# Kernel optimization log

Hardware: AMD Instinct MI355X
Metric: run time of the kernel (lower is better)

The kernel has to match this reference:

```python
import jax, jax.numpy as jnp
import numpy as np

B, WORDS, DIM = 16, 32, 256
HEADS, DIM_HEAD = 8, 32
INNER = HEADS * DIM_HEAD  # 256 == DIM -> project_out True
ITER = 3
J = WORDS * HEADS  # input capsules axis


def setup_inputs() -> dict:
    key = jax.random.key(0)
    ks = jax.random.split(key, 6)
    x = jax.random.normal(ks[0], (B, WORDS, DIM), jnp.float32)
    # capsule transform weights: [J, I, E, D] = [words*heads, words, inner, dim_head]
    W = jax.random.normal(ks[1], (J, WORDS, INNER, DIM_HEAD), jnp.float32)
    bias = 0.01 * jax.random.normal(ks[2], (J, WORDS, INNER), jnp.float32)
    Wi = jax.random.normal(ks[3], (INNER, DIM), jnp.float32) / np.sqrt(DIM)
    bi = jnp.zeros((INNER,), jnp.float32)
    Wo = jax.random.normal(ks[4], (DIM, INNER), jnp.float32) / np.sqrt(INNER)
    bo = jnp.zeros((DIM,), jnp.float32)
    return {"x": x, "W": W, "bias": bias, "Wi": Wi, "bi": bi, "Wo": Wo, "bo": bo}


def _squash(s):
    n = jnp.linalg.norm(s, axis=-1, keepdims=True)
    return n / (1.0 + n * n) * s


def reference(x, W, bias, Wi, bi, Wo, bo):
    # inner projection: [B, WORDS, INNER]
    xi = x @ Wi.T + bi
    # 'b n (h d) -> b (n h) d'
    xh = xi.reshape(B, WORDS * HEADS, DIM_HEAD)
    # u_hat[b,j,i,e] = sum_d W[j,i,e,d] * xh[b,j,d]  -> [B, J, WORDS, INNER]
    u_hat = jnp.einsum('jied,bjd->bjie', W, xh) + bias
    u_det = jax.lax.stop_gradient(u_hat)
    b_log = jnp.zeros_like(u_hat)
    v = None
    for i in range(ITER):
        c = jax.nn.softmax(b_log, axis=2)          # over output capsules (words)
        u = u_hat if i == ITER - 1 else u_det       # detach except last iter
        s = jnp.sum(c * u, axis=1, keepdims=True)   # [B,1,WORDS,INNER]
        v = _squash(s)
        if i < ITER - 1:
            b_log = b_log + jnp.sum(u_det * v, axis=3, keepdims=True)
    out = jnp.squeeze(v, 1) @ Wo.T + bo             # [B, WORDS, DIM]
    return out
```

## Files before the change

kernel.cpp:

```cpp
#include <hip/hip_runtime.h>

#define BB   16
#define NW   32
#define DIMM 256
#define DH   32
#define NI   256
#define NJ   256
#define JP   8
#define JG   (NJ / JP)

__global__ void k_proj_in(const float* __restrict__ x, const float* __restrict__ Wi,
                          const float* __restrict__ bi, float* __restrict__ xh) {
    int row = blockIdx.x;
    int k = threadIdx.x;
    __shared__ float xr[DIMM];
    xr[k] = x[(size_t)row * DIMM + k];
    __syncthreads();
    const float4* wi  = (const float4*)(Wi + (size_t)k * DIMM);
    const float4* xr4 = (const float4*)xr;
    float acc = bi[k];
#pragma unroll 8
    for (int m = 0; m < DIMM / 4; ++m) {
        float4 w = wi[m]; float4 xv = xr4[m];
        acc += w.x * xv.x + w.y * xv.y + w.z * xv.z + w.w * xv.w;
    }
    xh[(size_t)row * DIMM + k] = acc;
}

__global__ void k_uhat(const float* __restrict__ W, const float* __restrict__ bias,
                       const float* __restrict__ xh, float* __restrict__ u,
                       float* __restrict__ part) {
    int jg = blockIdx.x >> 5;
    int i  = blockIdx.x & 31;
    int e  = threadIdx.x;
    __shared__ float xs[BB][DH];
    float acc0[BB];
#pragma unroll
    for (int b = 0; b < BB; ++b) acc0[b] = 0.f;

    for (int jj = 0; jj < JP; ++jj) {
        int j = jg * JP + jj;
        __syncthreads();
        for (int t = threadIdx.x; t < BB * DH; t += 256) {
            int b = t >> 5, d = t & 31;
            xs[b][d] = xh[((size_t)b * NJ + j) * DH + d];
        }
        __syncthreads();
        const float4* wp = (const float4*)(W + (((size_t)j * NW + i) * NI + e) * DH);
        float4 w4[8];
#pragma unroll
        for (int q = 0; q < 8; ++q) w4[q] = wp[q];
        const float* w = (const float*)w4;
        float bv = bias[((size_t)j * NW + i) * NI + e];
#pragma unroll
        for (int b = 0; b < BB; ++b) {
            float a = bv;
#pragma unroll
            for (int d = 0; d < DH; ++d) a += w[d] * xs[b][d];
            u[(((size_t)b * NJ + j) * NW + i) * NI + e] = a;
            acc0[b] += a;
        }
    }
#pragma unroll
    for (int b = 0; b < BB; ++b)
        part[(((size_t)b * JG + jg) * NW + i) * NI + e] = acc0[b];
}

__global__ void k_route(const float* __restrict__ u, const float* __restrict__ v,
                        float* __restrict__ b_log, float* __restrict__ part, int accflag) {
    int b  = blockIdx.x / JG;
    int jg = blockIdx.x % JG;
    int tid = threadIdx.x;
    int lane = tid & 63, wave = tid >> 6;
    __shared__ float vs[NW][NI];
    __shared__ float red[NW][4];
    __shared__ float cs[NW];
    for (int t = tid; t < NW * NI; t += 256)
        vs[t >> 8][t & 255] = v[(size_t)b * NW * NI + t];
    __syncthreads();

    float s_acc[NW];
#pragma unroll
    for (int i = 0; i < NW; ++i) s_acc[i] = 0.f;

    for (int jj = 0; jj < JP; ++jj) {
        int j = jg * JP + jj;
        const float* up = u + ((size_t)b * NJ + j) * NW * NI;
        float ur[NW];
#pragma unroll
        for (int i = 0; i < NW; ++i) ur[i] = up[(size_t)i * NI + tid];
#pragma unroll
        for (int i = 0; i < NW; ++i) {
            float p = ur[i] * vs[i][tid];
#pragma unroll
            for (int off = 32; off >= 1; off >>= 1) p += __shfl_down(p, off);
            if (lane == 0) red[i][wave] = p;
        }
        __syncthreads();
        if (tid < NW) {
            float bta = red[tid][0] + red[tid][1] + red[tid][2] + red[tid][3];
            size_t bidx = ((size_t)b * NJ + j) * NW + tid;
            if (accflag) bta += b_log[bidx];
            b_log[bidx] = bta;
            float m = bta;
#pragma unroll
            for (int mask = 16; mask >= 1; mask >>= 1) m = fmaxf(m, __shfl_xor(m, mask));
            float ex = __expf(bta - m);
            float ssum = ex;
#pragma unroll
            for (int mask = 16; mask >= 1; mask >>= 1) ssum += __shfl_xor(ssum, mask);
            cs[tid] = ex / ssum;
        }
        __syncthreads();
#pragma unroll
        for (int i = 0; i < NW; ++i) s_acc[i] += cs[i] * ur[i];
    }
#pragma unroll
    for (int i = 0; i < NW; ++i)
        part[(((size_t)b * JG + jg) * NW + i) * NI + tid] = s_acc[i];
}

__global__ void k_reduce(const float* __restrict__ part, float* __restrict__ v,
                         float scale) {
    int b = blockIdx.x >> 5;
    int i = blockIdx.x & 31;
    int tid = threadIdx.x;
    int lane = tid & 63, wave = tid >> 6;
    float acc = 0.f;
#pragma unroll 8
    for (int g = 0; g < JG; ++g)
        acc += part[(((size_t)b * JG + g) * NW + i) * NI + tid];
    acc *= scale;
    __shared__ float red[4];
    float p = acc * acc;
#pragma unroll
    for (int off = 32; off >= 1; off >>= 1) p += __shfl_down(p, off);
    if (lane == 0) red[wave] = p;
    __syncthreads();
    float n2 = red[0] + red[1] + red[2] + red[3];
    float n = sqrtf(n2);
    float f = n / (1.0f + n2);
    v[((size_t)b * NW + i) * NI + tid] = f * acc;
}

__global__ void k_proj_out(const float* __restrict__ v, const float* __restrict__ Wo,
                           const float* __restrict__ bo, float* __restrict__ out) {
    int row = blockIdx.x;
    int k = threadIdx.x;
    __shared__ float vr[NI];
    vr[k] = v[(size_t)row * NI + k];
    __syncthreads();
    const float4* wo  = (const float4*)(Wo + (size_t)k * NI);
    const float4* vr4 = (const float4*)vr;
    float acc = bo[k];
#pragma unroll 8
    for (int m = 0; m < NI / 4; ++m) {
        float4 w = wo[m]; float4 xv = vr4[m];
        acc += w.x * xv.x + w.y * xv.y + w.z * xv.z + w.w * xv.w;
    }
    out[(size_t)row * DIMM + k] = acc;
}

extern "C" void kernel_launch(void* const* d_in, const int* in_sizes, int n_in,
                              void* d_out, int out_size, void* d_ws, size_t ws_size,
                              hipStream_t stream) {
    const float* x    = (const float*)d_in[0];
    const float* W    = (const float*)d_in[1];
    const float* bias = (const float*)d_in[2];
    const float* Wi   = (const float*)d_in[3];
    const float* bi   = (const float*)d_in[4];
    const float* Wo   = (const float*)d_in[5];
    const float* bo   = (const float*)d_in[6];
    float* out = (float*)d_out;

    float* ws    = (float*)d_ws;
    float* xh    = ws;
    float* u     = ws + 131072;
    float* part  = u + 33554432;
    float* b_log = part + 4194304;
    float* v     = b_log + 131072;

    k_proj_in<<<dim3(BB * NW), dim3(256), 0, stream>>>(x, Wi, bi, xh);
    k_uhat<<<dim3(JG * NW), dim3(256), 0, stream>>>(W, bias, xh, u, part);
    k_reduce<<<dim3(BB * NW), dim3(256), 0, stream>>>(part, v, 1.0f / NW);
    k_route<<<dim3(BB * JG), dim3(256), 0, stream>>>(u, v, b_log, part, 0);
    k_reduce<<<dim3(BB * NW), dim3(256), 0, stream>>>(part, v, 1.0f);
    k_route<<<dim3(BB * JG), dim3(256), 0, stream>>>(u, v, b_log, part, 1);
    k_reduce<<<dim3(BB * NW), dim3(256), 0, stream>>>(part, v, 1.0f);
    k_proj_out<<<dim3(BB * NW), dim3(256), 0, stream>>>(v, Wo, bo, out);
}
```

Baseline: 606.4 us.

## Remap routing threads to (capsule, slice) with vectorized loads and halve JP

The routing kernel now gives each thread a 32-element contiguous slice of one output capsule row. It loads u and v with float4 reads and reduces the dot product over only 8 lanes, replacing the per-capsule 64-wide wave reductions and the 32KB shared-memory copy of v. Every thread recomputes the softmax from shared beta values instead of one wave doing it, which removes one barrier per iteration. JP drops from 8 to 4 to double the number of blocks, which doubles the partial-sum buffer and the work in k_uhat and k_reduce, and the workspace offsets are shifted to match.

After: 579.8 us. 4.4% less time.

```diff
diff --git a/kernel.cpp b/kernel.cpp
--- a/kernel.cpp
+++ b/kernel.cpp
@@ -6,7 +6,7 @@
 #define DH   32
 #define NI   256
 #define NJ   256
-#define JP   8
+#define JP   4
 #define JG   (NJ / JP)
 
 __global__ void k_proj_in(const float* __restrict__ x, const float* __restrict__ Wi,
@@ -70,54 +70,59 @@
                         float* __restrict__ b_log, float* __restrict__ part, int accflag) {
     int b  = blockIdx.x / JG;
     int jg = blockIdx.x % JG;
-    int tid = threadIdx.x;
-    int lane = tid & 63, wave = tid >> 6;
-    __shared__ float vs[NW][NI];
-    __shared__ float red[NW][4];
-    __shared__ float cs[NW];
-    for (int t = tid; t < NW * NI; t += 256)
-        vs[t >> 8][t & 255] = v[(size_t)b * NW * NI + t];
-    __syncthreads();
+    int t  = threadIdx.x;
+    int i  = t >> 3;
+    int h  = t & 7;
+    __shared__ float sh_beta[JP][NW];
 
-    float s_acc[NW];
+    float vr[32];
+    {
+        const float4* vp = (const float4*)(v + ((size_t)b * NW + i) * NI + h * 32);
 #pragma unroll
-    for (int i = 0; i < NW; ++i) s_acc[i] = 0.f;
+        for (int q = 0; q < 8; ++q) ((float4*)vr)[q] = vp[q];
+    }
+    float s_acc[32];
+#pragma unroll
+    for (int k = 0; k < 32; ++k) s_acc[k] = 0.f;
 
     for (int jj = 0; jj < JP; ++jj) {
         int j = jg * JP + jj;
-        const float* up = u + ((size_t)b * NJ + j) * NW * NI;
-        float ur[NW];
+        float ur[32];
+        {
+            const float4* up = (const float4*)(u + (((size_t)b * NJ + j) * NW + i) * NI + h * 32);
 #pragma unroll
-        for (int i = 0; i < NW; ++i) ur[i] = up[(size_t)i * NI + tid];
+            for (int q = 0; q < 8; ++q) ((float4*)ur)[q] = up[q];
+        }
+        float p = 0.f;
 #pragma unroll
-        for (int i = 0; i < NW; ++i) {
-            float p = ur[i] * vs[i][tid];
-#pragma unroll
-            for (int off = 32; off >= 1; off >>= 1) p += __shfl_down(p, off);
-            if (lane == 0) red[i][wave] = p;
+        for (int k = 0; k < 32; ++k) p += ur[k] * vr[k];
+        p += __shfl_xor(p, 1);
+        p += __shfl_xor(p, 2);
+        p += __shfl_xor(p, 4);
+        if (h == 0) {
+            size_t bidx = ((size_t)b * NJ + j) * NW + i;
+            float bta = p;
+            if (accflag) bta += b_log[bidx];
+            b_log[bidx] = bta;
+            sh_beta[jj][i] = bta;
         }
         __syncthreads();
-        if (tid < NW) {
-            float bta = red[tid][0] + red[tid][1] + red[tid][2] + red[tid][3];
-            size_t bidx = ((size_t)b * NJ + j) * NW + tid;
-            if (accflag) bta += b_log[bidx];
-            b_log[bidx] = bta;
-            float m = bta;
+        float row[NW];
 #pragma unroll
-            for (int mask = 16; mask >= 1; mask >>= 1) m = fmaxf(m, __shfl_xor(m, mask));
-            float ex = __expf(bta - m);
-            float ssum = ex;
+        for (int k = 0; k < NW; ++k) row[k] = sh_beta[jj][k];
+        float m = row[0];
 #pragma unroll
-            for (int mask = 16; mask >= 1; mask >>= 1) ssum += __shfl_xor(ssum, mask);
-            cs[tid] = ex / ssum;
-        }
-        __syncthreads();
+        for (int k = 1; k < NW; ++k) m = fmaxf(m, row[k]);
+        float ssum = 0.f;
 #pragma unroll
-        for (int i = 0; i < NW; ++i) s_acc[i] += cs[i] * ur[i];
+        for (int k = 0; k < NW; ++k) ssum += __expf(row[k] - m);
+        float c = __expf(row[i] - m) / ssum;
+#pragma unroll
+        for (int k = 0; k < 32; ++k) s_acc[k] += c * ur[k];
     }
+    float4* pp = (float4*)(part + (((size_t)b * JG + jg) * NW + i) * NI + h * 32);
 #pragma unroll
-    for (int i = 0; i < NW; ++i)
-        part[(((size_t)b * JG + jg) * NW + i) * NI + tid] = s_acc[i];
+    for (int q = 0; q < 8; ++q) pp[q] = ((float4*)s_acc)[q];
 }
 
 __global__ void k_reduce(const float* __restrict__ part, float* __restrict__ v,
@@ -177,7 +182,7 @@
     float* xh    = ws;
     float* u     = ws + 131072;
     float* part  = u + 33554432;
-    float* b_log = part + 4194304;
+    float* b_log = part + 8388608;
     float* v     = b_log + 131072;
 
     k_proj_in<<<dim3(BB * NW), dim3(256), 0, stream>>>(x, Wi, bi, xh);
```
